# Kernel tuning notes

Measured on AMD Instinct MI355X. Metric: run time of the kernel, lower is better.

Reference implementation:

```python
import jax, jax.numpy as jnp
import numpy as np

N, D, DO, R, E, NV, K = 50000, 256, 256, 4, 500000, 10000, 8
EPS = 1e-8  # torch cosine_similarity eps


def setup_inputs() -> dict:
    key = jax.random.key(0)
    ks = jax.random.split(key, 7)
    x = jax.random.normal(ks[0], (N, D), jnp.float32)
    We = jax.random.normal(ks[1], (R, D, DO), jnp.float32) * (1.0 / np.sqrt(D))
    Wn = jax.random.normal(ks[2], (D, DO), jnp.float32) * (1.0 / np.sqrt(D))
    bn = jnp.zeros((DO,), jnp.float32)
    src = jax.random.randint(ks[3], (R, E), 0, N, jnp.int32)
    dst = jax.random.randint(ks[4], (R, E), 0, N, jnp.int32)
    candidates = jax.random.randint(ks[5], (NV, K), 0, NV, jnp.int32)
    return {"x": x, "We": We, "Wn": Wn, "bn": bn,
            "src": src, "dst": dst, "candidates": candidates, "n_vul": NV}


def reference(x, We, Wn, bn, src, dst, candidates, n_vul):
    n = x.shape[0]
    ht = x @ Wn + bn  # nweight projection (dst features) [N, DO]
    h_list, ma_list = [], []
    for r in range(We.shape[0]):  # small fixed set of relation types
        hr = x @ We[r]            # eweight projection, no bias [N, DO]
        hsrc = hr[src[r]]         # gather per-edge src features [E, DO]
        hdst = ht[dst[r]]         # gather per-edge dst features [E, DO]
        # cosine similarity edge attention
        num = jnp.sum(hsrc * hdst, axis=-1)
        den = (jnp.maximum(jnp.linalg.norm(hsrc, axis=-1), EPS)
               * jnp.maximum(jnp.linalg.norm(hdst, axis=-1), EPS))
        s = num / den             # [E]
        # reduce: h = sum_e a*h_src ; ma = mean_e a  (per dst node)
        hsum = jax.ops.segment_sum(s[:, None] * hsrc, dst[r], num_segments=n)
        asum = jax.ops.segment_sum(s, dst[r], num_segments=n)
        cnt = jax.ops.segment_sum(jnp.ones_like(s), dst[r], num_segments=n)
        ma_list.append(asum / jnp.maximum(cnt, 1.0))
        h_list.append(hsum)
    h = jnp.stack(h_list, axis=1)    # 'stack' cross-reducer -> [N, R, DO]
    ma = jnp.stack(ma_list, axis=1)  # [N, R]

    # AggregateLayer.edge_mask: pairwise candidate masking on entity ('vul') nodes
    Hv = h[:n_vul]                         # [NV, R, DO]
    diff = Hv[:, None] - Hv[candidates]    # [NV, K, R, DO]
    d2 = diff * diff
    att = jax.nn.softmax(-jnp.sqrt(jnp.sum(d2, axis=(2, 3))), axis=1)  # [NV, K]
    mask = jnp.exp(-jnp.einsum('nk,nkrd->nrd', att, d2))               # [NV, R, DO]
    h = jnp.concatenate([Hv * mask, h[n_vul:]], axis=0)

    # relation-axis softmax aggregation
    w = jax.nn.softmax(ma, axis=1)
    return jnp.einsum('nr,nrd->nd', w, h)  # [N, DO]
```

## Files before the change

### kernel.cpp

```cpp
#include <hip/hip_runtime.h>

#define N_NODES 50000
#define DIM     256
#define R_REL   4
#define E_EDGES 500000
#define NV_VUL  10000
#define K_CAND  8
#define EPS_C   1e-8f
#define RN      (R_REL * N_NODES)
#define NB      196
#define TB      (R_REL * NB)
#define BCAP    5120
#define EPB     4096

typedef short bf16x8 __attribute__((ext_vector_type(8)));
typedef float f32x4  __attribute__((ext_vector_type(4)));
typedef float f32x2  __attribute__((ext_vector_type(2)));
typedef unsigned short us8 __attribute__((ext_vector_type(8)));
typedef unsigned int u32x4 __attribute__((ext_vector_type(4)));

__device__ __forceinline__ unsigned short f2bf_rne(float f) {
  unsigned u = __builtin_bit_cast(unsigned, f);
  unsigned r = (u + 0x7FFFu + ((u >> 16) & 1u)) >> 16;
  return (unsigned short)r;
}
__device__ __forceinline__ float bf2f(unsigned short h) {
  unsigned u = ((unsigned)h) << 16;
  return __builtin_bit_cast(float, u);
}
__device__ __forceinline__ f32x2 expand_bf2(unsigned dw) {
  f32x2 v;
  v.x = __builtin_bit_cast(float, dw << 16);
  v.y = __builtin_bit_cast(float, dw & 0xFFFF0000u);
  return v;
}

__global__ __launch_bounds__(256) void k_convert_x(const float* __restrict__ x,
                                                   unsigned short* __restrict__ x16) {
  const int total = N_NODES * DIM / 8;
  for (int i = blockIdx.x * blockDim.x + threadIdx.x; i < total;
       i += gridDim.x * blockDim.x) {
    float4 a = *(const float4*)(x + (size_t)i * 8);
    float4 b = *(const float4*)(x + (size_t)i * 8 + 4);
    us8 o;
    o[0] = f2bf_rne(a.x); o[1] = f2bf_rne(a.y); o[2] = f2bf_rne(a.z); o[3] = f2bf_rne(a.w);
    o[4] = f2bf_rne(b.x); o[5] = f2bf_rne(b.y); o[6] = f2bf_rne(b.z); o[7] = f2bf_rne(b.w);
    *(us8*)(x16 + (size_t)i * 8) = o;
  }
}

__global__ __launch_bounds__(256) void k_convert_w(const float* __restrict__ Wn,
                                                   const float* __restrict__ We,
                                                   short* __restrict__ Bthi) {
  __shared__ float tile[64][65];
  int w  = blockIdx.z;
  int k0 = blockIdx.x * 64, n0 = blockIdx.y * 64;
  const float* W = (w == 0) ? Wn : We + (size_t)(w - 1) * 65536;
  int tx = threadIdx.x & 63, ty = threadIdx.x >> 6;
  for (int i = ty; i < 64; i += 4)
    tile[i][tx] = W[(size_t)(k0 + i) * 256 + n0 + tx];
  __syncthreads();
  for (int i = ty; i < 64; i += 4) {
    float f = tile[tx][i];
    size_t o = (size_t)w * 65536 + (size_t)(n0 + i) * 256 + k0 + tx;
    Bthi[o] = (short)f2bf_rne(f);
  }
}

#define GBM 128
#define GBK 32
__global__ __launch_bounds__(512) void k_gemm_all(const unsigned short* __restrict__ A16,
                                                  const short* __restrict__ Bthi_all,
                                                  const float* __restrict__ bnb,
                                                  unsigned short* __restrict__ ht16,
                                                  unsigned short* __restrict__ hr0,
                                                  unsigned short* __restrict__ hr1,
                                                  unsigned short* __restrict__ hr2,
                                                  unsigned short* __restrict__ hr3,
                                                  float* __restrict__ nrm_sq_all,
                                                  int M) {
  __shared__ short Ahi_s[128][GBK + 8];
  __shared__ short Bhi_s[256][GBK + 8];
  const int w = blockIdx.z;
  const short* Bthi = Bthi_all + (size_t)w * 65536;
  unsigned short* C16 = (w == 0) ? ht16 : (w == 1) ? hr0 : (w == 2) ? hr1 : (w == 3) ? hr2 : hr3;
  const float* bias = (w == 0) ? bnb : nullptr;
  float* nrm_sq = nrm_sq_all + (size_t)w * N_NODES;

  const int t    = threadIdx.x;
  const int bm0  = blockIdx.x * GBM;
  const int wave = t >> 6, lane = t & 63;
  const int wm   = (wave >> 2) * 64;
  const int wn   = (wave & 3) * 64;
  const int m16  = lane & 15, kg = lane >> 4;

  f32x4 acc[4][4] = {};

  const int arow = t >> 2, ac = t & 3;
  int agrow = bm0 + arow; if (agrow >= M) agrow = M - 1;
  const unsigned short* aptr = A16 + (size_t)agrow * 256 + ac * 8;
  const int brow0 = t >> 2, bc = t & 3;

  for (int k0 = 0; k0 < DIM; k0 += GBK) {
    *(us8*)&Ahi_s[arow][ac * 8] = *(const us8*)(aptr + k0);
    *(bf16x8*)&Bhi_s[brow0][bc * 8] =
        *(const bf16x8*)(Bthi + (size_t)brow0 * 256 + k0 + bc * 8);
    *(bf16x8*)&Bhi_s[brow0 + 128][bc * 8] =
        *(const bf16x8*)(Bthi + (size_t)(brow0 + 128) * 256 + k0 + bc * 8);
    __syncthreads();

    bf16x8 ah[4], bh[4];
#pragma unroll
    for (int i = 0; i < 4; i++) {
      ah[i] = *(const bf16x8*)&Ahi_s[wm + i * 16 + m16][kg * 8];
      bh[i] = *(const bf16x8*)&Bhi_s[wn + i * 16 + m16][kg * 8];
    }
#pragma unroll
    for (int mi = 0; mi < 4; mi++)
#pragma unroll
      for (int ni = 0; ni < 4; ni++)
        acc[mi][ni] = __builtin_amdgcn_mfma_f32_16x16x32_bf16(ah[mi], bh[ni], acc[mi][ni], 0, 0, 0);
    __syncthreads();
  }

#pragma unroll
  for (int mi = 0; mi < 4; mi++) {
    float ps[4] = {0.f, 0.f, 0.f, 0.f};
#pragma unroll
    for (int ni = 0; ni < 4; ni++) {
      int col = wn + ni * 16 + m16;
      float bb = bias ? bias[col] : 0.f;
      f32x4 v = acc[mi][ni];
#pragma unroll
      for (int j = 0; j < 4; j++) {
        float vj = v[j] + bb;
        int row = bm0 + wm + mi * 16 + kg * 4 + j;
        if (row < M) C16[(size_t)row * 256 + col] = f2bf_rne(vj);
        ps[j] += vj * vj;
      }
    }
#pragma unroll
    for (int j = 0; j < 4; j++) {
      float s = ps[j];
      s += __shfl_xor(s, 1);
      s += __shfl_xor(s, 2);
      s += __shfl_xor(s, 4);
      s += __shfl_xor(s, 8);
      if (m16 == 0) {
        int row = bm0 + wm + mi * 16 + kg * 4 + j;
        if (row < M) atomicAdd(&nrm_sq[row], s);
      }
    }
  }
}

__global__ __launch_bounds__(256) void k_rnorm(float* __restrict__ sq) {
  int i = blockIdx.x * blockDim.x + threadIdx.x;
  if (i < 5 * N_NODES) sq[i] = fminf(rsqrtf(sq[i]), 1e8f);
}

__global__ __launch_bounds__(1024) void k_bin(const int* __restrict__ src,
                                              const int* __restrict__ dst,
                                              int* __restrict__ cursor,
                                              int* __restrict__ binned) {
  __shared__ int hist[TB];
  __shared__ int base[TB];
  int tid = threadIdx.x;
  for (int i = tid; i < TB; i += 1024) hist[i] = 0;
  __syncthreads();
  int e0 = blockIdx.x * EPB;
  int myb[4], myrank[4], myp[4];
#pragma unroll
  for (int i = 0; i < 4; i++) {
    int e = e0 + i * 1024 + tid;
    myb[i] = -1;
    if (e < R_REL * E_EDGES) {
      int r = e / E_EDGES;
      int d = dst[e];
      int s = src[e];
      int b = r * NB + (d >> 8);
      myb[i]    = b;
      myp[i]    = (s << 8) | (d & 255);
      myrank[i] = atomicAdd(&hist[b], 1);
    }
  }
  __syncthreads();
  for (int i = tid; i < TB; i += 1024) {
    int c = hist[i];
    base[i] = c ? atomicAdd(&cursor[i], c) : 0;
  }
  __syncthreads();
#pragma unroll
  for (int i = 0; i < 4; i++) {
    if (myb[i] >= 0) {
      int pos = base[myb[i]] + myrank[i];
      if (pos < BCAP) binned[(size_t)myb[i] * BCAP + pos] = myp[i];
    }
  }
}

__global__ __launch_bounds__(1024) void k_bucket_scan(const int* __restrict__ cnt,
                                                      int* __restrict__ bbase,
                                                      int* __restrict__ offsets) {
  __shared__ int s[1024];
  int tid = threadIdx.x;
  int v = (tid < TB) ? cnt[tid] : 0;
  s[tid] = v;
  __syncthreads();
  for (int off = 1; off < 1024; off <<= 1) {
    int t2 = (tid >= off) ? s[tid - off] : 0;
    __syncthreads();
    s[tid] += t2;
    __syncthreads();
  }
  if (tid < TB) bbase[tid] = s[tid] - v;
  if (tid == TB - 1) offsets[RN] = s[tid];
}

__global__ __launch_bounds__(256) void k_csr(const int* __restrict__ binned,
                                             const int* __restrict__ cnt_arr,
                                             const int* __restrict__ bbase,
                                             int* __restrict__ offsets,
                                             int* __restrict__ edge_src) {
  __shared__ int hist[256];
  __shared__ int excl[256];
  int b   = blockIdx.x;
  int tid = threadIdx.x;
  int cnt = cnt_arr[b]; if (cnt > BCAP) cnt = BCAP;
  int gbase = bbase[b];
  hist[tid] = 0;
  __syncthreads();
  const int* bp = binned + (size_t)b * BCAP;
  for (int i = tid; i < cnt; i += 256) atomicAdd(&hist[bp[i] & 255], 1);
  __syncthreads();
  int v = hist[tid];
  excl[tid] = v;
  __syncthreads();
  for (int off = 1; off < 256; off <<= 1) {
    int t2 = (tid >= off) ? excl[tid - off] : 0;
    __syncthreads();
    excl[tid] += t2;
    __syncthreads();
  }
  int ex = excl[tid] - v;
  int r = b / NB, bloc = b % NB;
  int node = bloc * 256 + tid;
  if (node < N_NODES) offsets[r * N_NODES + node] = gbase + ex;
  hist[tid] = gbase + ex;
  __syncthreads();
  for (int i = tid; i < cnt; i += 256) {
    int p = bp[i];
    int pos = atomicAdd(&hist[p & 255], 1);
    edge_src[pos] = p >> 8;
  }
}

__global__ __launch_bounds__(256) void k_aggregate_fused(
    const unsigned short* __restrict__ hr0, const unsigned short* __restrict__ hr1,
    const unsigned short* __restrict__ hr2, const unsigned short* __restrict__ hr3,
    const unsigned short* __restrict__ ht16, const float* __restrict__ rn,
    const int* __restrict__ offsets, const int* __restrict__ edge_src,
    unsigned short* __restrict__ h16, float* __restrict__ ma,
    float* __restrict__ out) {
  int n    = (int)((blockIdx.x * (size_t)blockDim.x + threadIdx.x) >> 6);
  int lane = threadIdx.x & 63;
  if (n >= N_NODES) return;
  int g = lane >> 4, l16 = lane & 15;

  const u32x4* htp = (const u32x4*)(ht16 + (size_t)n * DIM + l16 * 16);
  u32x4 hta = __builtin_nontemporal_load(htp);
  u32x4 htb = __builtin_nontemporal_load(htp + 1);
  float rd = rn[n];
  f32x2 rd2 = {rd, rd};
  f32x2 hd2[8];
  hd2[0] = expand_bf2(hta[0]) * rd2; hd2[1] = expand_bf2(hta[1]) * rd2;
  hd2[2] = expand_bf2(hta[2]) * rd2; hd2[3] = expand_bf2(hta[3]) * rd2;
  hd2[4] = expand_bf2(htb[0]) * rd2; hd2[5] = expand_bf2(htb[1]) * rd2;
  hd2[6] = expand_bf2(htb[2]) * rd2; hd2[7] = expand_bf2(htb[3]) * rd2;

  const unsigned short* hr = (g == 0) ? hr0 : (g == 1) ? hr1 : (g == 2) ? hr2 : hr3;
  const float* nq = rn + (size_t)(1 + g) * N_NODES;
  int b   = offsets[g * N_NODES + n];
  int end = offsets[g * N_NODES + n + 1];

  f32x2 acc2[8] = {};
  float asum = 0.f;

  auto loadslot = [&](int i, uint4& ua, uint4& ub, float& q) {
    if (i < end) {
      int sn = edge_src[i];
      const uint4* rp = (const uint4*)(hr + (size_t)sn * DIM + l16 * 16);
      ua = rp[0]; ub = rp[1];
      q  = nq[sn];
    }
  };
  auto consume = [&](uint4 ua, uint4 ub, float q, bool valid) {
    f32x2 hs2[8];
    hs2[0] = expand_bf2(ua.x); hs2[1] = expand_bf2(ua.y);
    hs2[2] = expand_bf2(ua.z); hs2[3] = expand_bf2(ua.w);
    hs2[4] = expand_bf2(ub.x); hs2[5] = expand_bf2(ub.y);
    hs2[6] = expand_bf2(ub.z); hs2[7] = expand_bf2(ub.w);
    f32x2 d2 = hs2[0] * hd2[0];
#pragma unroll
    for (int i = 1; i < 8; i++) d2 += hs2[i] * hd2[i];
    float num = d2.x + d2.y;
    num += __shfl_xor(num, 1);
    num += __shfl_xor(num, 2);
    num += __shfl_xor(num, 4);
    num += __shfl_xor(num, 8);
    float s = valid ? num * q : 0.f;
    f32x2 s2 = {s, s};
#pragma unroll
    for (int i = 0; i < 8; i++) acc2[i] += hs2[i] * s2;
    asum += s;
  };

  uint4 uaA = {0,0,0,0}, ubA = {0,0,0,0}, uaB = {0,0,0,0}, ubB = {0,0,0,0};
  float qA = 1.f, qB = 1.f;
  loadslot(b,     uaA, ubA, qA);
  loadslot(b + 1, uaB, ubB, qB);
  for (int i = b; i < end; i += 2) {
    uint4 uaC = {0,0,0,0}, ubC = {0,0,0,0}, uaD = {0,0,0,0}, ubD = {0,0,0,0};
    float qC = 1.f, qD = 1.f;
    loadslot(i + 2, uaC, ubC, qC);
    loadslot(i + 3, uaD, ubD, qD);
    consume(uaA, ubA, qA, true);
    consume(uaB, ubB, qB, (i + 1) < end);
    uaA = uaC; ubA = ubC; qA = qC;
    uaB = uaD; ubB = ubD; qB = qD;
  }

  float mymean = asum / fmaxf((float)(end - b), 1.0f);

  if (n < NV_VUL) {
    us8 o1, o2;
#pragma unroll
    for (int i = 0; i < 4; i++) {
      o1[2 * i]     = f2bf_rne(acc2[i].x);
      o1[2 * i + 1] = f2bf_rne(acc2[i].y);
      o2[2 * i]     = f2bf_rne(acc2[4 + i].x);
      o2[2 * i + 1] = f2bf_rne(acc2[4 + i].y);
    }
    unsigned short* hp = h16 + ((size_t)n * R_REL + g) * DIM + l16 * 16;
    *(us8*)hp       = o1;
    *(us8*)(hp + 8) = o2;
    if (l16 == 0) ma[n * R_REL + g] = mymean;
  } else {
    float a1 = __shfl_xor(mymean, 16);
    float a2 = __shfl_xor(mymean, 32);
    float a3 = __shfl_xor(mymean, 48);
    float mx = fmaxf(fmaxf(mymean, a1), fmaxf(a2, a3));
    float e0 = expf(mymean - mx);
    float denom = e0 + expf(a1 - mx) + expf(a2 - mx) + expf(a3 - mx);
    float w = e0 / denom;
    f32x2 o[8];
#pragma unroll
    for (int i = 0; i < 8; i++) {
      f32x2 v = acc2[i] * (f32x2){w, w};
      v.x += __shfl_xor(v.x, 16); v.x += __shfl_xor(v.x, 32);
      v.y += __shfl_xor(v.y, 16); v.y += __shfl_xor(v.y, 32);
      o[i] = v;
    }
    if (g == 0) {
      float* op = out + (size_t)n * 256 + l16 * 16;
      f32x4 v0 = {o[0].x, o[0].y, o[1].x, o[1].y};
      f32x4 v1 = {o[2].x, o[2].y, o[3].x, o[3].y};
      f32x4 v2 = {o[4].x, o[4].y, o[5].x, o[5].y};
      f32x4 v3 = {o[6].x, o[6].y, o[7].x, o[7].y};
      __builtin_nontemporal_store(v0, (f32x4*)(op + 0));
      __builtin_nontemporal_store(v1, (f32x4*)(op + 4));
      __builtin_nontemporal_store(v2, (f32x4*)(op + 8));
      __builtin_nontemporal_store(v3, (f32x4*)(op + 12));
    }
  }
}

__global__ __launch_bounds__(256) void k_vuln_combine(const unsigned short* __restrict__ h16,
                                                      const int* __restrict__ cand,
                                                      const float* __restrict__ ma,
                                                      float* __restrict__ out) {
  __shared__ float red[8][4];
  __shared__ float dist2s[8];
  __shared__ float sm[1024];
  int n   = blockIdx.x;
  int tid = threadIdx.x;
  ushort4 hb = *(const ushort4*)(h16 + (size_t)n * 1024 + tid * 4);
  float4 hv;
  hv.x = bf2f(hb.x); hv.y = bf2f(hb.y); hv.z = bf2f(hb.z); hv.w = bf2f(hb.w);
  float4 d2[8];
  int wid = tid >> 6, lane = tid & 63;
#pragma unroll
  for (int k = 0; k < 8; k++) {
    int c = cand[n * 8 + k];
    ushort4 cb = *(const ushort4*)(h16 + (size_t)c * 1024 + tid * 4);
    float4 df;
    df.x = hv.x - bf2f(cb.x); df.y = hv.y - bf2f(cb.y);
    df.z = hv.z - bf2f(cb.z); df.w = hv.w - bf2f(cb.w);
    d2[k].x = df.x * df.x; d2[k].y = df.y * df.y;
    d2[k].z = df.z * df.z; d2[k].w = df.w * df.w;
    float v = d2[k].x + d2[k].y + d2[k].z + d2[k].w;
    for (int off = 32; off; off >>= 1) v += __shfl_xor(v, off);
    if (lane == 0) red[k][wid] = v;
  }
  __syncthreads();
  if (tid < 32) {
    int k = tid >> 2, w2 = tid & 3;
    float v = red[k][w2];
    v += __shfl_xor(v, 1, 4);
    v += __shfl_xor(v, 2, 4);
    if (w2 == 0) dist2s[k] = v;
  }
  __syncthreads();
  float dk[8], mn = 1e30f;
#pragma unroll
  for (int k = 0; k < 8; k++) { dk[k] = sqrtf(dist2s[k]); mn = fminf(mn, dk[k]); }
  float se = 0.f, att[8];
#pragma unroll
  for (int k = 0; k < 8; k++) { att[k] = expf(mn - dk[k]); se += att[k]; }
  float inv = 1.f / se;
  float4 accv = {0.f, 0.f, 0.f, 0.f};
#pragma unroll
  for (int k = 0; k < 8; k++) {
    float a = att[k] * inv;
    accv.x += a * d2[k].x; accv.y += a * d2[k].y;
    accv.z += a * d2[k].z; accv.w += a * d2[k].w;
  }
  float m0 = ma[n * 4 + 0], m1 = ma[n * 4 + 1], m2 = ma[n * 4 + 2], m3 = ma[n * 4 + 3];
  float mx = fmaxf(fmaxf(m0, m1), fmaxf(m2, m3));
  float w0 = expf(m0 - mx), w1 = expf(m1 - mx), w2f = expf(m2 - mx), w3 = expf(m3 - mx);
  float winv = 1.f / (w0 + w1 + w2f + w3);
  float wr = (tid < 64) ? w0 : (tid < 128) ? w1 : (tid < 192) ? w2f : w3;
  float c = wr * winv;
  float4 o;
  o.x = c * hv.x * expf(-accv.x);
  o.y = c * hv.y * expf(-accv.y);
  o.z = c * hv.z * expf(-accv.z);
  o.w = c * hv.w * expf(-accv.w);
  *(float4*)&sm[tid * 4] = o;
  __syncthreads();
  if (tid < 256) {
    float v = sm[tid] + sm[256 + tid] + sm[512 + tid] + sm[768 + tid];
    __builtin_nontemporal_store(v, out + (size_t)n * 256 + tid);
  }
}

__global__ void k_fallback(float* __restrict__ out, int out_size, float wsmb) {
  int i = blockIdx.x * blockDim.x + threadIdx.x;
  if (i < out_size) out[i] = (i == 0) ? wsmb : 0.f;
}

extern "C" void kernel_launch(void* const* d_in, const int* in_sizes, int n_in,
                              void* d_out, int out_size, void* d_ws, size_t ws_size,
                              hipStream_t stream) {
  const float* x   = (const float*)d_in[0];
  const float* We  = (const float*)d_in[1];
  const float* Wn  = (const float*)d_in[2];
  const float* bnb = (const float*)d_in[3];
  const int* src   = (const int*)d_in[4];
  const int* dst   = (const int*)d_in[5];
  const int* cand  = (const int*)d_in[6];
  float* out = (float*)d_out;

  char* ws = (char*)d_ws;
  size_t off = 0;
  auto alloc = [&](size_t bytes) -> void* {
    void* p = ws + off;
    off += (bytes + 255) & ~(size_t)255;
    return p;
  };
  unsigned short* ht16        = (unsigned short*)alloc((size_t)N_NODES * DIM * 2);
  unsigned short* h16         = (unsigned short*)alloc((size_t)NV_VUL * R_REL * DIM * 2);
  float*          ma          = (float*)alloc((size_t)NV_VUL * R_REL * 4);
  float*          nsq         = (float*)alloc((size_t)5 * N_NODES * 4);
  int*            bucket_cnt  = (int*)alloc((size_t)TB * 4);
  int*            bucket_base = (int*)alloc((size_t)TB * 4);
  int*            offsets     = (int*)alloc((size_t)(RN + 1) * 4);
  int*            edge_src    = (int*)alloc((size_t)R_REL * E_EDGES * 4);
  short*          Bthi        = (short*)alloc((size_t)5 * 65536 * 2);
  unsigned short* x16         = (unsigned short*)alloc((size_t)N_NODES * DIM * 2);
  unsigned short* hr0         = (unsigned short*)alloc((size_t)N_NODES * DIM * 2);
  unsigned short* hr1         = (unsigned short*)alloc((size_t)N_NODES * DIM * 2);
  unsigned short* hr2         = (unsigned short*)alloc((size_t)N_NODES * DIM * 2);
  unsigned short* hr3         = (unsigned short*)alloc((size_t)N_NODES * DIM * 2);
  size_t required = off;
  (void)in_sizes; (void)n_in;

  if (ws_size < required) {
    k_fallback<<<(out_size + 255) / 256, 256, 0, stream>>>(out, out_size,
                                                           (float)(ws_size >> 20));
    return;
  }

  int* binned = (int*)h16;

  hipMemsetAsync(bucket_cnt, 0, (size_t)TB * 4, stream);
  hipMemsetAsync(nsq, 0, (size_t)5 * N_NODES * 4, stream);

  k_convert_w<<<dim3(4, 4, 5), 256, 0, stream>>>(Wn, We, Bthi);
  k_convert_x<<<2048, 256, 0, stream>>>(x, x16);

  k_bin<<<(R_REL * E_EDGES + EPB - 1) / EPB, 1024, 0, stream>>>(src, dst, bucket_cnt, binned);
  k_bucket_scan<<<1, 1024, 0, stream>>>(bucket_cnt, bucket_base, offsets);
  k_csr<<<TB, 256, 0, stream>>>(binned, bucket_cnt, bucket_base, offsets, edge_src);

  dim3 gemm_grid((N_NODES + GBM - 1) / GBM, 1, 5);
  k_gemm_all<<<gemm_grid, 512, 0, stream>>>(x16, Bthi, bnb, ht16, hr0, hr1, hr2, hr3,
                                            nsq, N_NODES);

  k_rnorm<<<(5 * N_NODES + 255) / 256, 256, 0, stream>>>(nsq);
  k_aggregate_fused<<<(N_NODES * 64 + 255) / 256, 256, 0, stream>>>(
      hr0, hr1, hr2, hr3, ht16, nsq, offsets, edge_src, h16, ma, out);

  k_vuln_combine<<<NV_VUL, 256, 0, stream>>>(h16, cand, ma, out);
}
```

Baseline: 359.1 us.

## Fuse prep kernels into one launch and compute inverse norms inside GEMM

The weight transpose/convert, x conversion and edge binning kernels are merged into one k_prep launch that splits its blocks by role. The GEMM now accumulates row squared norms in shared memory and writes the clamped reciprocal sqrt directly. This drops the nsq memset, the k_rnorm kernel and the global atomics. The intent is to cut launch overhead and serialization between small kernels. In exchange, the conversion blocks now use 1024 threads, and the prep kernel carries the binning kernel's shared-memory footprint for every block.

```diff
diff --git a/kernel.cpp b/kernel.cpp
--- a/kernel.cpp
+++ b/kernel.cpp
@@ -12,6 +12,9 @@
 #define TB      (R_REL * NB)
 #define BCAP    5120
 #define EPB     4096
+#define PREP_W   80
+#define PREP_X   128
+#define PREP_BIN ((R_REL * E_EDGES + EPB - 1) / EPB)
 
 typedef short bf16x8 __attribute__((ext_vector_type(8)));
 typedef float f32x4  __attribute__((ext_vector_type(4)));
@@ -35,140 +38,53 @@
   return v;
 }
 
-__global__ __launch_bounds__(256) void k_convert_x(const float* __restrict__ x,
-                                                   unsigned short* __restrict__ x16) {
-  const int total = N_NODES * DIM / 8;
-  for (int i = blockIdx.x * blockDim.x + threadIdx.x; i < total;
-       i += gridDim.x * blockDim.x) {
-    float4 a = *(const float4*)(x + (size_t)i * 8);
-    float4 b = *(const float4*)(x + (size_t)i * 8 + 4);
-    us8 o;
-    o[0] = f2bf_rne(a.x); o[1] = f2bf_rne(a.y); o[2] = f2bf_rne(a.z); o[3] = f2bf_rne(a.w);
-    o[4] = f2bf_rne(b.x); o[5] = f2bf_rne(b.y); o[6] = f2bf_rne(b.z); o[7] = f2bf_rne(b.w);
-    *(us8*)(x16 + (size_t)i * 8) = o;
-  }
-}
-
-__global__ __launch_bounds__(256) void k_convert_w(const float* __restrict__ Wn,
-                                                   const float* __restrict__ We,
-                                                   short* __restrict__ Bthi) {
+__global__ __launch_bounds__(1024) void k_prep(const float* __restrict__ x,
+                                               const float* __restrict__ Wn,
+                                               const float* __restrict__ We,
+                                               unsigned short* __restrict__ x16,
+                                               short* __restrict__ Bthi,
+                                               const int* __restrict__ src,
+                                               const int* __restrict__ dst,
+                                               int* __restrict__ cursor,
+                                               int* __restrict__ binned) {
   __shared__ float tile[64][65];
-  int w  = blockIdx.z;
-  int k0 = blockIdx.x * 64, n0 = blockIdx.y * 64;
-  const float* W = (w == 0) ? Wn : We + (size_t)(w - 1) * 65536;
-  int tx = threadIdx.x & 63, ty = threadIdx.x >> 6;
-  for (int i = ty; i < 64; i += 4)
-    tile[i][tx] = W[(size_t)(k0 + i) * 256 + n0 + tx];
-  __syncthreads();
-  for (int i = ty; i < 64; i += 4) {
-    float f = tile[tx][i];
-    size_t o = (size_t)w * 65536 + (size_t)(n0 + i) * 256 + k0 + tx;
-    Bthi[o] = (short)f2bf_rne(f);
-  }
-}
-
-#define GBM 128
-#define GBK 32
-__global__ __launch_bounds__(512) void k_gemm_all(const unsigned short* __restrict__ A16,
-                                                  const short* __restrict__ Bthi_all,
-                                                  const float* __restrict__ bnb,
-                                                  unsigned short* __restrict__ ht16,
-                                                  unsigned short* __restrict__ hr0,
-                                                  unsigned short* __restrict__ hr1,
-                                                  unsigned short* __restrict__ hr2,
-                                                  unsigned short* __restrict__ hr3,
-                                                  float* __restrict__ nrm_sq_all,
-                                                  int M) {
-  __shared__ short Ahi_s[128][GBK + 8];
-  __shared__ short Bhi_s[256][GBK + 8];
-  const int w = blockIdx.z;
-  const short* Bthi = Bthi_all + (size_t)w * 65536;
-  unsigned short* C16 = (w == 0) ? ht16 : (w == 1) ? hr0 : (w == 2) ? hr1 : (w == 3) ? hr2 : hr3;
-  const float* bias = (w == 0) ? bnb : nullptr;
-  float* nrm_sq = nrm_sq_all + (size_t)w * N_NODES;
-
-  const int t    = threadIdx.x;
-  const int bm0  = blockIdx.x * GBM;
-  const int wave = t >> 6, lane = t & 63;
-  const int wm   = (wave >> 2) * 64;
-  const int wn   = (wave & 3) * 64;
-  const int m16  = lane & 15, kg = lane >> 4;
-
-  f32x4 acc[4][4] = {};
-
-  const int arow = t >> 2, ac = t & 3;
-  int agrow = bm0 + arow; if (agrow >= M) agrow = M - 1;
-  const unsigned short* aptr = A16 + (size_t)agrow * 256 + ac * 8;
-  const int brow0 = t >> 2, bc = t & 3;
-
-  for (int k0 = 0; k0 < DIM; k0 += GBK) {
-    *(us8*)&Ahi_s[arow][ac * 8] = *(const us8*)(aptr + k0);
-    *(bf16x8*)&Bhi_s[brow0][bc * 8] =
-        *(const bf16x8*)(Bthi + (size_t)brow0 * 256 + k0 + bc * 8);
-    *(bf16x8*)&Bhi_s[brow0 + 128][bc * 8] =
-        *(const bf16x8*)(Bthi + (size_t)(brow0 + 128) * 256 + k0 + bc * 8);
-    __syncthreads();
-
-    bf16x8 ah[4], bh[4];
-#pragma unroll
-    for (int i = 0; i < 4; i++) {
-      ah[i] = *(const bf16x8*)&Ahi_s[wm + i * 16 + m16][kg * 8];
-      bh[i] = *(const bf16x8*)&Bhi_s[wn + i * 16 + m16][kg * 8];
-    }
-#pragma unroll
-    for (int mi = 0; mi < 4; mi++)
-#pragma unroll
-      for (int ni = 0; ni < 4; ni++)
-        acc[mi][ni] = __builtin_amdgcn_mfma_f32_16x16x32_bf16(ah[mi], bh[ni], acc[mi][ni], 0, 0, 0);
-    __syncthreads();
-  }
-
-#pragma unroll
-  for (int mi = 0; mi < 4; mi++) {
-    float ps[4] = {0.f, 0.f, 0.f, 0.f};
-#pragma unroll
-    for (int ni = 0; ni < 4; ni++) {
-      int col = wn + ni * 16 + m16;
-      float bb = bias ? bias[col] : 0.f;
-      f32x4 v = acc[mi][ni];
-#pragma unroll
-      for (int j = 0; j < 4; j++) {
-        float vj = v[j] + bb;
-        int row = bm0 + wm + mi * 16 + kg * 4 + j;
-        if (row < M) C16[(size_t)row * 256 + col] = f2bf_rne(vj);
-        ps[j] += vj * vj;
-      }
-    }
-#pragma unroll
-    for (int j = 0; j < 4; j++) {
-      float s = ps[j];
-      s += __shfl_xor(s, 1);
-      s += __shfl_xor(s, 2);
-      s += __shfl_xor(s, 4);
-      s += __shfl_xor(s, 8);
-      if (m16 == 0) {
-        int row = bm0 + wm + mi * 16 + kg * 4 + j;
-        if (row < M) atomicAdd(&nrm_sq[row], s);
-      }
-    }
-  }
-}
-
-__global__ __launch_bounds__(256) void k_rnorm(float* __restrict__ sq) {
-  int i = blockIdx.x * blockDim.x + threadIdx.x;
-  if (i < 5 * N_NODES) sq[i] = fminf(rsqrtf(sq[i]), 1e8f);
-}
-
-__global__ __launch_bounds__(1024) void k_bin(const int* __restrict__ src,
-                                              const int* __restrict__ dst,
-                                              int* __restrict__ cursor,
-                                              int* __restrict__ binned) {
   __shared__ int hist[TB];
   __shared__ int base[TB];
+  int blk = blockIdx.x;
   int tid = threadIdx.x;
+
+  if (blk < PREP_W) {
+    int w   = blk / 16;
+    int rem = blk % 16;
+    int k0  = (rem / 4) * 64, n0 = (rem % 4) * 64;
+    const float* W = (w == 0) ? Wn : We + (size_t)(w - 1) * 65536;
+    int tx = tid & 63, ty = tid >> 6;
+    for (int i = ty; i < 64; i += 16)
+      tile[i][tx] = W[(size_t)(k0 + i) * 256 + n0 + tx];
+    __syncthreads();
+    for (int i = ty; i < 64; i += 16) {
+      float f = tile[tx][i];
+      size_t o = (size_t)w * 65536 + (size_t)(n0 + i) * 256 + k0 + tx;
+      Bthi[o] = (short)f2bf_rne(f);
+    }
+    return;
+  }
+  if (blk < PREP_W + PREP_X) {
+    const int total = N_NODES * DIM / 8;
+    for (int i = (blk - PREP_W) * 1024 + tid; i < total; i += PREP_X * 1024) {
+      float4 a = *(const float4*)(x + (size_t)i * 8);
+      float4 b = *(const float4*)(x + (size_t)i * 8 + 4);
+      us8 o;
+      o[0] = f2bf_rne(a.x); o[1] = f2bf_rne(a.y); o[2] = f2bf_rne(a.z); o[3] = f2bf_rne(a.w);
+      o[4] = f2bf_rne(b.x); o[5] = f2bf_rne(b.y); o[6] = f2bf_rne(b.z); o[7] = f2bf_rne(b.w);
+      *(us8*)(x16 + (size_t)i * 8) = o;
+    }
+    return;
+  }
+  int bb = blk - PREP_W - PREP_X;
   for (int i = tid; i < TB; i += 1024) hist[i] = 0;
   __syncthreads();
-  int e0 = blockIdx.x * EPB;
+  int e0 = bb * EPB;
   int myb[4], myrank[4], myp[4];
 #pragma unroll
   for (int i = 0; i < 4; i++) {
@@ -196,6 +112,98 @@
       int pos = base[myb[i]] + myrank[i];
       if (pos < BCAP) binned[(size_t)myb[i] * BCAP + pos] = myp[i];
     }
+  }
+}
+
+#define GBM 128
+#define GBK 32
+__global__ __launch_bounds__(512) void k_gemm_all(const unsigned short* __restrict__ A16,
+                                                  const short* __restrict__ Bthi_all,
+                                                  const float* __restrict__ bnb,
+                                                  unsigned short* __restrict__ ht16,
+                                                  unsigned short* __restrict__ hr0,
+                                                  unsigned short* __restrict__ hr1,
+                                                  unsigned short* __restrict__ hr2,
+                                                  unsigned short* __restrict__ hr3,
+                                                  float* __restrict__ rn_all,
+                                                  int M) {
+  __shared__ short Ahi_s[128][GBK + 8];
+  __shared__ short Bhi_s[256][GBK + 8];
+  __shared__ float nsq_s[128];
+  const int w = blockIdx.z;
+  const short* Bthi = Bthi_all + (size_t)w * 65536;
+  unsigned short* C16 = (w == 0) ? ht16 : (w == 1) ? hr0 : (w == 2) ? hr1 : (w == 3) ? hr2 : hr3;
+  const float* bias = (w == 0) ? bnb : nullptr;
+  float* rn = rn_all + (size_t)w * N_NODES;
+
+  const int t    = threadIdx.x;
+  const int bm0  = blockIdx.x * GBM;
+  const int wave = t >> 6, lane = t & 63;
+  const int wm   = (wave >> 2) * 64;
+  const int wn   = (wave & 3) * 64;
+  const int m16  = lane & 15, kg = lane >> 4;
+
+  if (t < 128) nsq_s[t] = 0.f;
+
+  f32x4 acc[4][4] = {};
+
+  const int arow = t >> 2, ac = t & 3;
+  int agrow = bm0 + arow; if (agrow >= M) agrow = M - 1;
+  const unsigned short* aptr = A16 + (size_t)agrow * 256 + ac * 8;
+  const int brow0 = t >> 2, bc = t & 3;
+
+  for (int k0 = 0; k0 < DIM; k0 += GBK) {
+    *(us8*)&Ahi_s[arow][ac * 8] = *(const us8*)(aptr + k0);
+    *(bf16x8*)&Bhi_s[brow0][bc * 8] =
+        *(const bf16x8*)(Bthi + (size_t)brow0 * 256 + k0 + bc * 8);
+    *(bf16x8*)&Bhi_s[brow0 + 128][bc * 8] =
+        *(const bf16x8*)(Bthi + (size_t)(brow0 + 128) * 256 + k0 + bc * 8);
+    __syncthreads();
+
+    bf16x8 ah[4], bh[4];
+#pragma unroll
+    for (int i = 0; i < 4; i++) {
+      ah[i] = *(const bf16x8*)&Ahi_s[wm + i * 16 + m16][kg * 8];
+      bh[i] = *(const bf16x8*)&Bhi_s[wn + i * 16 + m16][kg * 8];
+    }
+#pragma unroll
+    for (int mi = 0; mi < 4; mi++)
+#pragma unroll
+      for (int ni = 0; ni < 4; ni++)
+        acc[mi][ni] = __builtin_amdgcn_mfma_f32_16x16x32_bf16(ah[mi], bh[ni], acc[mi][ni], 0, 0, 0);
+    __syncthreads();
+  }
+
+#pragma unroll
+  for (int mi = 0; mi < 4; mi++) {
+    float ps[4] = {0.f, 0.f, 0.f, 0.f};
+#pragma unroll
+    for (int ni = 0; ni < 4; ni++) {
+      int col = wn + ni * 16 + m16;
+      float bb = bias ? bias[col] : 0.f;
+      f32x4 v = acc[mi][ni];
+#pragma unroll
+      for (int j = 0; j < 4; j++) {
+        float vj = v[j] + bb;
+        int row = bm0 + wm + mi * 16 + kg * 4 + j;
+        if (row < M) C16[(size_t)row * 256 + col] = f2bf_rne(vj);
+        ps[j] += vj * vj;
+      }
+    }
+#pragma unroll
+    for (int j = 0; j < 4; j++) {
+      float s = ps[j];
+      s += __shfl_xor(s, 1);
+      s += __shfl_xor(s, 2);
+      s += __shfl_xor(s, 4);
+      s += __shfl_xor(s, 8);
+      if (m16 == 0) atomicAdd(&nsq_s[wm + mi * 16 + kg * 4 + j], s);
+    }
+  }
+  __syncthreads();
+  if (t < 128) {
+    int row = bm0 + t;
+    if (row < M) rn[row] = fminf(rsqrtf(nsq_s[t]), 1e8f);
   }
 }
 
@@ -471,7 +479,7 @@
   unsigned short* ht16        = (unsigned short*)alloc((size_t)N_NODES * DIM * 2);
   unsigned short* h16         = (unsigned short*)alloc((size_t)NV_VUL * R_REL * DIM * 2);
   float*          ma          = (float*)alloc((size_t)NV_VUL * R_REL * 4);
-  float*          nsq         = (float*)alloc((size_t)5 * N_NODES * 4);
+  float*          rn          = (float*)alloc((size_t)5 * N_NODES * 4);
   int*            bucket_cnt  = (int*)alloc((size_t)TB * 4);
   int*            bucket_base = (int*)alloc((size_t)TB * 4);
   int*            offsets     = (int*)alloc((size_t)(RN + 1) * 4);
@@ -494,22 +502,18 @@
   int* binned = (int*)h16;
 
   hipMemsetAsync(bucket_cnt, 0, (size_t)TB * 4, stream);
-  hipMemsetAsync(nsq, 0, (size_t)5 * N_NODES * 4, stream);
-
-  k_convert_w<<<dim3(4, 4, 5), 256, 0, stream>>>(Wn, We, Bthi);
-  k_convert_x<<<2048, 256, 0, stream>>>(x, x16);
-
-  k_bin<<<(R_REL * E_EDGES + EPB - 1) / EPB, 1024, 0, stream>>>(src, dst, bucket_cnt, binned);
+
+  k_prep<<<PREP_W + PREP_X + PREP_BIN, 1024, 0, stream>>>(x, Wn, We, x16, Bthi,
+                                                          src, dst, bucket_cnt, binned);
   k_bucket_scan<<<1, 1024, 0, stream>>>(bucket_cnt, bucket_base, offsets);
   k_csr<<<TB, 256, 0, stream>>>(binned, bucket_cnt, bucket_base, offsets, edge_src);
 
   dim3 gemm_grid((N_NODES + GBM - 1) / GBM, 1, 5);
   k_gemm_all<<<gemm_grid, 512, 0, stream>>>(x16, Bthi, bnb, ht16, hr0, hr1, hr2, hr3,
-                                            nsq, N_NODES);
-
-  k_rnorm<<<(5 * N_NODES + 255) / 256, 256, 0, stream>>>(nsq);
+                                            rn, N_NODES);
+
   k_aggregate_fused<<<(N_NODES * 64 + 255) / 256, 256, 0, stream>>>(
-      hr0, hr1, hr2, hr3, ht16, nsq, offsets, edge_src, h16, ma, out);
+      hr0, hr1, hr2, hr3, ht16, rn, offsets, edge_src, h16, ma, out);
 
   k_vuln_combine<<<NV_VUL, 256, 0, stream>>>(h16, cand, ma, out);
 }
```

Measured after the change: 336.2 us (median of 2 runs). 1.07x faster.
